# Optimization experiments

Hardware: AMD Instinct MI355X
Metric: run time of the kernel (lower is better)

## Reference

```python
import jax, jax.numpy as jnp
import numpy as np

B, S, D = 4, 2048, 1024          # batch, seq, hidden_units
E, K, I = 16, 2, 1024            # n_routed_experts, top_k, moe_inter_dim
SH = 2                            # n_shared_experts -> shared inter = SH*I
ROUTE_SCALE = 1.0


def setup_inputs() -> dict:
    key = jax.random.key(0)
    ks = jax.random.split(key, 12)
    std = 0.02
    return {
        "x": jax.random.normal(ks[0], (B, S, D), jnp.float32),
        "gate_w": jax.random.normal(ks[1], (E, D), jnp.float32) * std,
        # expert weights, torch Linear layout [out, in], stacked over experts
        "w1": jax.random.normal(ks[2], (E, I, D), jnp.float32) * std,
        "w2": jax.random.normal(ks[3], (E, D, I), jnp.float32) * std,
        "w3": jax.random.normal(ks[4], (E, I, D), jnp.float32) * std,
        # shared expert MLP (bias=True, nn.Linear default)
        "sw1": jax.random.normal(ks[5], (SH * I, D), jnp.float32) * std,
        "sb1": jnp.zeros((SH * I,), jnp.float32),
        "sw2": jax.random.normal(ks[6], (D, SH * I), jnp.float32) * std,
        "sb2": jnp.zeros((D,), jnp.float32),
        "sw3": jax.random.normal(ks[7], (SH * I, D), jnp.float32) * std,
        "sb3": jnp.zeros((SH * I,), jnp.float32),
    }


def reference(x, gate_w, w1, w2, w3, sw1, sb1, sw2, sb2, sw3, sb3):
    orig_shape = x.shape
    xt = x.reshape(-1, D)                       # [T, D]
    T = xt.shape[0]

    # ---- Gate: sigmoid scores, top-k, normalized weights ----
    scores = jax.nn.sigmoid(xt @ gate_w.T)      # [T, E]
    topk_vals, topk_idx = jax.lax.top_k(scores, K)
    weights = topk_vals / topk_vals.sum(-1, keepdims=True) * ROUTE_SCALE  # [T, K]

    # dense per-token-per-expert combine weight (zero for unselected experts)
    onehot = jax.nn.one_hot(topk_idx, E, dtype=xt.dtype)  # [T, K, E]
    w_full = jnp.einsum('tk,tke->te', weights, onehot)    # [T, E]

    # ---- Routed experts: SwiGLU per expert, weighted combine ----
    y = jnp.zeros_like(xt)
    for e in range(E):  # fixed small structural loop over experts
        h = jax.nn.silu(xt @ w1[e].T) * (xt @ w3[e].T)    # [T, I]
        y = y + w_full[:, e:e + 1] * (h @ w2[e].T)

    # ---- Load-balancing auxiliary loss ----
    counts = jax.lax.stop_gradient(onehot.sum((0, 1)))    # tokens per expert (non-diff, as in torch)
    expert_probs = w_full.sum(0)                          # sum of routing weights per expert
    f_i = E * counts / (K * T)
    P_i = expert_probs / T
    L_ExpBal = (f_i * P_i).sum()

    # ---- Shared expert (dense SwiGLU MLP with bias) ----
    z = (jax.nn.silu(xt @ sw1.T + sb1) * (xt @ sw3.T + sb3)) @ sw2.T + sb2

    return (y + z).reshape(orig_shape), L_ExpBal
```

## Files before the change

kernel.cpp:

```cpp
#include <hip/hip_runtime.h>
#include <cstdint>
#include <cstddef>

typedef unsigned short ushort_t;
typedef __attribute__((ext_vector_type(8))) short bf16x8;
typedef __attribute__((ext_vector_type(8))) unsigned short u16x8;
typedef __attribute__((ext_vector_type(4))) float f32x4;

#define T_TOKENS 8192
#define DIM      1024
#define NEXP     16

static __device__ __forceinline__ unsigned short f2bf(float f) {
  union { float f; unsigned u; } v; v.f = f;
  unsigned r = v.u + 0x7FFFu + ((v.u >> 16) & 1u);
  return (unsigned short)(r >> 16);
}

static __device__ __forceinline__ void gload16(const void* g, void* l) {
  __builtin_amdgcn_global_load_lds(
      (const __attribute__((address_space(1))) unsigned int*)g,
      (__attribute__((address_space(3))) unsigned int*)l, 16, 0, 0);
}

static __device__ __forceinline__ void xcd_map(int bx, int by, int gy,
                                               int& rb, int& cb) {
  int lin = bx + (by << 6);
  int xcd = lin & 7;
  int c = lin >> 3;
  int gyd = gy >> 3;
  cb = xcd * gyd + (c >> 6);
  rb = c & 63;
}

__global__ __launch_bounds__(256) void k_cvt8(const float* __restrict__ in,
                                              ushort_t* __restrict__ outp) {
  size_t i = ((size_t)blockIdx.x * 256 + threadIdx.x) * 8;
  float4 a = *(const float4*)(in + i);
  float4 b = *(const float4*)(in + i + 4);
  u16x8 o;
  o[0]=f2bf(a.x); o[1]=f2bf(a.y); o[2]=f2bf(a.z); o[3]=f2bf(a.w);
  o[4]=f2bf(b.x); o[5]=f2bf(b.y); o[6]=f2bf(b.z); o[7]=f2bf(b.w);
  *(u16x8*)(outp + i) = o;
}

__global__ __launch_bounds__(64) void k_score(const float* __restrict__ x,
                                              const float* __restrict__ gw,
                                              int* __restrict__ sel0,
                                              int* __restrict__ sel1,
                                              float* __restrict__ w0o,
                                              float* __restrict__ w1o) {
  int t = blockIdx.x;
  int lane = threadIdx.x;
  float xv[16];
  const float* xr = x + (size_t)t * DIM + lane * 16;
#pragma unroll
  for (int j = 0; j < 16; j += 4) {
    float4 v = *(const float4*)(xr + j);
    xv[j] = v.x; xv[j+1] = v.y; xv[j+2] = v.z; xv[j+3] = v.w;
  }
  float sc[NEXP];
#pragma unroll
  for (int e = 0; e < NEXP; e++) {
    const float* gr = gw + (size_t)e * DIM + lane * 16;
    float a = 0.f;
#pragma unroll
    for (int j = 0; j < 16; j += 4) {
      float4 g = *(const float4*)(gr + j);
      a += xv[j]*g.x + xv[j+1]*g.y + xv[j+2]*g.z + xv[j+3]*g.w;
    }
#pragma unroll
    for (int o = 32; o > 0; o >>= 1) a += __shfl_xor(a, o, 64);
    sc[e] = 1.f / (1.f + expf(-a));
  }
  if (lane == 0) {
    float best = -1e30f, sec = -1e30f;
    int bi = 0, si = 0;
#pragma unroll
    for (int e = 0; e < NEXP; e++) {
      float s = sc[e];
      if (s > best) { sec = best; si = bi; best = s; bi = e; }
      else if (s > sec) { sec = s; si = e; }
    }
    float inv = 1.f / (best + sec);
    sel0[t] = bi; sel1[t] = si;
    w0o[t] = best * inv; w1o[t] = sec * inv;
  }
}

__global__ __launch_bounds__(256) void k_compact(const int* __restrict__ sel0,
                                                 const int* __restrict__ sel1,
                                                 const float* __restrict__ w0v,
                                                 const float* __restrict__ w1v,
                                                 int* __restrict__ toklist,
                                                 float* __restrict__ wlist,
                                                 int* __restrict__ cnt,
                                                 float* __restrict__ probs) {
  const int e = blockIdx.x;
  const int tid = threadIdx.x;
  const int lane = tid & 63, wv = tid >> 6;
  __shared__ int wbase[4];
  __shared__ int woff[4];
  __shared__ int base;
  __shared__ float pacc[4];
  if (tid == 0) base = 0;
  float myprob = 0.f;
  int* tl = toklist + e * T_TOKENS;
  float* wl = wlist + e * T_TOKENS;
  __syncthreads();
  for (int t0 = 0; t0 < T_TOKENS; t0 += 256) {
    int t = t0 + tid;
    bool m0 = (sel0[t] == e), m1 = (sel1[t] == e);
    bool m = m0 || m1;
    float wgt = m0 ? w0v[t] : (m1 ? w1v[t] : 0.f);
    unsigned long long bal = __ballot(m);
    int prefix = __popcll(bal & ((1ull << lane) - 1ull));
    if (lane == 0) wbase[wv] = __popcll(bal);
    __syncthreads();
    if (tid == 0) {
      int a = base;
#pragma unroll
      for (int i = 0; i < 4; i++) { woff[i] = a; a += wbase[i]; }
      base = a;
    }
    __syncthreads();
    if (m) {
      int pos = woff[wv] + prefix;
      tl[pos] = t;
      wl[pos] = wgt;
    }
    myprob += wgt;
  }
#pragma unroll
  for (int o = 32; o > 0; o >>= 1) myprob += __shfl_xor(myprob, o, 64);
  if (lane == 0) pacc[wv] = myprob;
  __syncthreads();
  if (tid == 0) {
    cnt[e] = base;
    probs[e] = pacc[0] + pacc[1] + pacc[2] + pacc[3];
  }
}

__global__ void k_offsets(const int* __restrict__ cnt, const float* __restrict__ probs,
                          int* __restrict__ seg, float* __restrict__ loss_out) {
  if (threadIdx.x == 0 && blockIdx.x == 0) {
    int acc = 0;
    float L = 0.f;
    for (int e = 0; e < NEXP; e++) {
      seg[e] = acc; acc += cnt[e];
      float f = 16.f * (float)cnt[e] / (2.f * 8192.f);
      L += f * (probs[e] / 8192.f);
    }
    seg[NEXP] = acc;
    *loss_out = L;
  }
}

__global__ __launch_bounds__(256, 3) void k_gemm1(
    const ushort_t* __restrict__ X,
    const ushort_t* __restrict__ W1b, const ushort_t* __restrict__ W3b,
    const float* __restrict__ b1, const float* __restrict__ b3,
    ushort_t* __restrict__ P, int ldP,
    const int* __restrict__ toklist, const int* __restrict__ cnt,
    const int* __restrict__ seg) {
  __shared__ __align__(16) ushort_t As[2 * 4096];
  __shared__ __align__(16) ushort_t B1s[2 * 2048];
  __shared__ __align__(16) ushort_t B3s[2 * 2048];

  const int tid = threadIdx.x;
  const int lane = tid & 63, wave = tid >> 6;
  const int wm = wave >> 1, wn = wave & 1;
  int rb, cb;
  xcd_map(blockIdx.x, blockIdx.y, gridDim.y, rb, cb);
  const int e = blockIdx.z;

  int Ne, pbase;
  const int* tl = nullptr;
  const ushort_t* W1 = W1b;
  const ushort_t* W3 = W3b;
  if (cnt) {
    Ne = cnt[e];
    if (rb * 128 >= Ne) return;
    pbase = seg[e];
    tl = toklist + e * T_TOKENS;
    W1 += (size_t)e * 1024 * 1024;
    W3 += (size_t)e * 1024 * 1024;
  } else { Ne = T_TOKENS; pbase = 0; }

  const int c0 = wave * 2, c1 = c0 + 1;
  const int lrow = lane >> 2;
  const int lcol = (lane & 3) * 8;

  const int ar0 = rb * 128 + c0 * 16 + lrow;
  const int ar1 = rb * 128 + c1 * 16 + lrow;
  const int sr0 = tl ? tl[min(ar0, Ne - 1)] : ar0;
  const int sr1 = tl ? tl[min(ar1, Ne - 1)] : ar1;
  const ushort_t* apA0 = X + (size_t)sr0 * DIM + lcol;
  const ushort_t* apA1 = X + (size_t)sr1 * DIM + lcol;

  const int brw = cb * 64 + wave * 16 + lrow;
  const ushort_t* bp1 = W1 + (size_t)brw * DIM + lcol;
  const ushort_t* bp3 = W3 + (size_t)brw * DIM + lcol;

  const int o0 = c0 * 512, o1 = c1 * 512;
  const int ow = wave * 512;

  f32x4 acc1[4][2], acc3[4][2];
#pragma unroll
  for (int m = 0; m < 4; m++)
#pragma unroll
    for (int n = 0; n < 2; n++) {
      acc1[m][n] = (f32x4){0.f, 0.f, 0.f, 0.f};
      acc3[m][n] = (f32x4){0.f, 0.f, 0.f, 0.f};
    }

  const int koff = (lane >> 4) * 8;

#define STAGE1(AB, BB, K0) { \
    gload16(apA0 + (K0), As  + (AB) + o0); \
    gload16(apA1 + (K0), As  + (AB) + o1); \
    gload16(bp1  + (K0), B1s + (BB) + ow); \
    gload16(bp3  + (K0), B3s + (BB) + ow); }

#define PHASE1(AC, BC, T, STG) { \
    if (STG) STAGE1(4096 - (AC), 2048 - (BC), ((T) + 1) * 32); \
    bf16x8 af[4], b1f[2], b3f[2]; \
    _Pragma("unroll") \
    for (int m = 0; m < 4; m++) { \
      int row = wm * 64 + m * 16 + (lane & 15); \
      af[m] = *(const bf16x8*)(As + (AC) + row * 32 + koff); } \
    _Pragma("unroll") \
    for (int n = 0; n < 2; n++) { \
      int rw = wn * 32 + n * 16 + (lane & 15); \
      b1f[n] = *(const bf16x8*)(B1s + (BC) + rw * 32 + koff); \
      b3f[n] = *(const bf16x8*)(B3s + (BC) + rw * 32 + koff); } \
    _Pragma("unroll") \
    for (int m = 0; m < 4; m++) \
      _Pragma("unroll") \
      for (int n = 0; n < 2; n++) { \
        acc1[m][n] = __builtin_amdgcn_mfma_f32_16x16x32_bf16(af[m], b1f[n], acc1[m][n], 0, 0, 0); \
        acc3[m][n] = __builtin_amdgcn_mfma_f32_16x16x32_bf16(af[m], b3f[n], acc3[m][n], 0, 0, 0); } \
    __syncthreads(); }

  STAGE1(0, 0, 0);
  __syncthreads();
  for (int kk = 0; kk < 30; kk += 2) {
    PHASE1(0, 0, kk, 1);
    PHASE1(4096, 2048, kk + 1, 1);
  }
  PHASE1(0, 0, 30, 1);
  PHASE1(4096, 2048, 31, 0);
#undef PHASE1
#undef STAGE1

#pragma unroll
  for (int n = 0; n < 2; n++) {
    int col = cb * 64 + wn * 32 + n * 16 + (lane & 15);
    float bb1 = b1 ? b1[col] : 0.f;
    float bb3 = b3 ? b3[col] : 0.f;
#pragma unroll
    for (int m = 0; m < 4; m++) {
#pragma unroll
      for (int r = 0; r < 4; r++) {
        int row = rb * 128 + wm * 64 + m * 16 + (lane >> 4) * 4 + r;
        if (row < Ne) {
          float h1 = acc1[m][n][r] + bb1;
          float h3 = acc3[m][n][r] + bb3;
          float pv = (h1 / (1.f + expf(-h1))) * h3;
          P[(size_t)(pbase + row) * ldP + col] = f2bf(pv);
        }
      }
    }
  }
}

__global__ __launch_bounds__(256, 3) void k_gemm2(
    const ushort_t* __restrict__ Pbuf, const ushort_t* __restrict__ W2b,
    const float* __restrict__ b2,
    float* __restrict__ outp,
    const int* __restrict__ toklist, const float* __restrict__ wlist,
    const int* __restrict__ cnt, const int* __restrict__ seg, int Kd) {
  __shared__ __align__(16) ushort_t As[2 * 4096];
  __shared__ __align__(16) ushort_t Bs[2 * 4096];

  const int tid = threadIdx.x;
  const int lane = tid & 63, wave = tid >> 6;
  const int wm = wave >> 1, wn = wave & 1;
  int rb, cb;
  xcd_map(blockIdx.x, blockIdx.y, gridDim.y, rb, cb);
  const int e = blockIdx.z;

  int Ne;
  const ushort_t* A;
  const ushort_t* W2 = W2b;
  const int* tl = nullptr; const float* wl = nullptr;
  if (cnt) {
    Ne = cnt[e];
    if (rb * 128 >= Ne) return;
    A = Pbuf + (size_t)seg[e] * Kd;
    W2 += (size_t)e * 1024 * Kd;
    tl = toklist + e * T_TOKENS;
    wl = wlist + e * T_TOKENS;
  } else { Ne = T_TOKENS; A = Pbuf; }

  const int c0 = wave * 2, c1 = c0 + 1;
  const int lrow = lane >> 2;
  const int lcol = (lane & 3) * 8;

  const int sr0 = min(rb * 128 + c0 * 16 + lrow, Ne - 1);
  const int sr1 = min(rb * 128 + c1 * 16 + lrow, Ne - 1);
  const ushort_t* apA0 = A + (size_t)sr0 * Kd + lcol;
  const ushort_t* apA1 = A + (size_t)sr1 * Kd + lcol;

  const int br0 = cb * 128 + c0 * 16 + lrow;
  const int br1 = cb * 128 + c1 * 16 + lrow;
  const ushort_t* bp0 = W2 + (size_t)br0 * Kd + lcol;
  const ushort_t* bp1 = W2 + (size_t)br1 * Kd + lcol;

  const int o0 = c0 * 512, o1 = c1 * 512;

  f32x4 acc[4][4];
#pragma unroll
  for (int m = 0; m < 4; m++)
#pragma unroll
    for (int n = 0; n < 4; n++) acc[m][n] = (f32x4){0.f, 0.f, 0.f, 0.f};

  const int koff = (lane >> 4) * 8;
  const int ksteps = Kd >> 5;

#define STAGE2(BUF, K0) { \
    gload16(apA0 + (K0), As + (BUF) + o0); \
    gload16(apA1 + (K0), As + (BUF) + o1); \
    gload16(bp0  + (K0), Bs + (BUF) + o0); \
    gload16(bp1  + (K0), Bs + (BUF) + o1); }

#define PHASE2(CUR, T, STG) { \
    if (STG) STAGE2(4096 - (CUR), ((T) + 1) * 32); \
    bf16x8 af[4], bf[4]; \
    _Pragma("unroll") \
    for (int m = 0; m < 4; m++) { \
      int row = wm * 64 + m * 16 + (lane & 15); \
      af[m] = *(const bf16x8*)(As + (CUR) + row * 32 + koff); } \
    _Pragma("unroll") \
    for (int n = 0; n < 4; n++) { \
      int rw = wn * 64 + n * 16 + (lane & 15); \
      bf[n] = *(const bf16x8*)(Bs + (CUR) + rw * 32 + koff); } \
    _Pragma("unroll") \
    for (int m = 0; m < 4; m++) \
      _Pragma("unroll") \
      for (int n = 0; n < 4; n++) \
        acc[m][n] = __builtin_amdgcn_mfma_f32_16x16x32_bf16(af[m], bf[n], acc[m][n], 0, 0, 0); \
    __syncthreads(); }

  STAGE2(0, 0);
  __syncthreads();
  for (int kk = 0; kk < ksteps - 2; kk += 2) {
    PHASE2(0, kk, 1);
    PHASE2(4096, kk + 1, 1);
  }
  PHASE2(0, ksteps - 2, 1);
  PHASE2(4096, ksteps - 1, 0);
#undef PHASE2
#undef STAGE2

#pragma unroll
  for (int n = 0; n < 4; n++) {
    int col = cb * 128 + wn * 64 + n * 16 + (lane & 15);
    float bias = b2 ? b2[col] : 0.f;
#pragma unroll
    for (int m = 0; m < 4; m++) {
#pragma unroll
      for (int r = 0; r < 4; r++) {
        int rl = rb * 128 + wm * 64 + m * 16 + (lane >> 4) * 4 + r;
        if (cnt) {
          if (rl < Ne) {
            int tok = tl[rl];
            float wgt = wl[rl];
            atomicAdd(outp + (size_t)tok * DIM + col, acc[m][n][r] * wgt);
          }
        } else {
          outp[(size_t)rl * DIM + col] = acc[m][n][r] + bias;
        }
      }
    }
  }
}

extern "C" void kernel_launch(void* const* d_in, const int* in_sizes, int n_in,
                              void* d_out, int out_size, void* d_ws, size_t ws_size,
                              hipStream_t stream) {
  const float* x   = (const float*)d_in[0];
  const float* gw  = (const float*)d_in[1];
  const float* w1  = (const float*)d_in[2];
  const float* w2  = (const float*)d_in[3];
  const float* w3  = (const float*)d_in[4];
  const float* sw1 = (const float*)d_in[5];
  const float* sb1 = (const float*)d_in[6];
  const float* sw2 = (const float*)d_in[7];
  const float* sb2 = (const float*)d_in[8];
  const float* sw3 = (const float*)d_in[9];
  const float* sb3 = (const float*)d_in[10];
  float* out  = (float*)d_out;
  float* loss = out + (size_t)T_TOKENS * DIM;

  const size_t NW = (size_t)NEXP * 1024 * 1024;
  const size_t NS = (size_t)2048 * 1024;

  char* w = (char*)d_ws;
  ushort_t* w1b  = (ushort_t*)w; w += NW * 2;
  ushort_t* w2b  = (ushort_t*)w; w += NW * 2;
  ushort_t* w3b  = (ushort_t*)w; w += NW * 2;
  ushort_t* sw1b = (ushort_t*)w; w += NS * 2;
  ushort_t* sw2b = (ushort_t*)w; w += NS * 2;
  ushort_t* sw3b = (ushort_t*)w; w += NS * 2;
  ushort_t* p_buf = (ushort_t*)w; w += (size_t)33554432 + 262144;
  ushort_t* x_bf  = (ushort_t*)w; w += (size_t)T_TOKENS * DIM * 2;
  int*   toklist  = (int*)w;      w += (size_t)NEXP * T_TOKENS * 4;
  float* wlist    = (float*)w;    w += (size_t)NEXP * T_TOKENS * 4;
  int*   sel0     = (int*)w;      w += (size_t)T_TOKENS * 4;
  int*   sel1     = (int*)w;      w += (size_t)T_TOKENS * 4;
  float* w0v      = (float*)w;    w += (size_t)T_TOKENS * 4;
  float* w1v      = (float*)w;    w += (size_t)T_TOKENS * 4;
  int*   cnt      = (int*)w;      w += 64;
  float* probs    = (float*)w;    w += 64;
  int*   seg      = (int*)w;      w += 128;

  k_cvt8<<<(T_TOKENS * DIM) / 2048, 256, 0, stream>>>(x, x_bf);
  k_cvt8<<<NW / 2048, 256, 0, stream>>>(w1, w1b);
  k_cvt8<<<NW / 2048, 256, 0, stream>>>(w2, w2b);
  k_cvt8<<<NW / 2048, 256, 0, stream>>>(w3, w3b);
  k_cvt8<<<NS / 2048, 256, 0, stream>>>(sw1, sw1b);
  k_cvt8<<<NS / 2048, 256, 0, stream>>>(sw2, sw2b);
  k_cvt8<<<NS / 2048, 256, 0, stream>>>(sw3, sw3b);

  k_score<<<T_TOKENS, 64, 0, stream>>>(x, gw, sel0, sel1, w0v, w1v);
  k_compact<<<NEXP, 256, 0, stream>>>(sel0, sel1, w0v, w1v,
                                      toklist, wlist, cnt, probs);
  k_offsets<<<1, 64, 0, stream>>>(cnt, probs, seg, loss);

  k_gemm1<<<dim3(64, 32, 1), 256, 0, stream>>>(x_bf, sw1b, sw3b, sb1, sb3,
                                               p_buf, 2048, nullptr, nullptr, nullptr);
  k_gemm2<<<dim3(64, 8, 1), 256, 0, stream>>>(p_buf, sw2b, sb2, out,
                                              nullptr, nullptr, nullptr, nullptr, 2048);

  k_gemm1<<<dim3(64, 16, NEXP), 256, 0, stream>>>(x_bf, w1b, w3b, nullptr, nullptr,
                                                  p_buf, 1024, toklist, cnt, seg);
  k_gemm2<<<dim3(64, 8, NEXP), 256, 0, stream>>>(p_buf, w2b, nullptr, out,
                                                 toklist, wlist, cnt, seg, 1024);
}
```

Baseline: 599.1 us.

## Double GEMM K-tile to 64 with XOR-swizzled LDS and batch score tokens per block

Both GEMM kernels now stage 64-wide K tiles instead of 32, so each tile is consumed in two MFMA half-steps per barrier. This halves the number of __syncthreads and pipeline iterations. The LDS layout gains an XOR swizzle on the 16-byte column chunk to avoid bank conflicts on the wider rows. LDS use doubles, so the occupancy hint drops from 3 to 2 blocks per CU. Separately, the scoring kernel packs four tokens (one per wave) into each 256-thread block, which cuts the launch block count.

```diff
diff --git a/kernel.cpp b/kernel.cpp
--- a/kernel.cpp
+++ b/kernel.cpp
@@ -44,14 +44,15 @@
   *(u16x8*)(outp + i) = o;
 }
 
-__global__ __launch_bounds__(64) void k_score(const float* __restrict__ x,
-                                              const float* __restrict__ gw,
-                                              int* __restrict__ sel0,
-                                              int* __restrict__ sel1,
-                                              float* __restrict__ w0o,
-                                              float* __restrict__ w1o) {
-  int t = blockIdx.x;
-  int lane = threadIdx.x;
+__global__ __launch_bounds__(256) void k_score(const float* __restrict__ x,
+                                               const float* __restrict__ gw,
+                                               int* __restrict__ sel0,
+                                               int* __restrict__ sel1,
+                                               float* __restrict__ w0o,
+                                               float* __restrict__ w1o) {
+  int lane = threadIdx.x & 63;
+  int wv = threadIdx.x >> 6;
+  int t = blockIdx.x * 4 + wv;
   float xv[16];
   const float* xr = x + (size_t)t * DIM + lane * 16;
 #pragma unroll
@@ -156,16 +157,17 @@
   }
 }
 
-__global__ __launch_bounds__(256, 3) void k_gemm1(
+
+__global__ __launch_bounds__(256, 2) void k_gemm1(
     const ushort_t* __restrict__ X,
     const ushort_t* __restrict__ W1b, const ushort_t* __restrict__ W3b,
     const float* __restrict__ b1, const float* __restrict__ b3,
     ushort_t* __restrict__ P, int ldP,
     const int* __restrict__ toklist, const int* __restrict__ cnt,
     const int* __restrict__ seg) {
-  __shared__ __align__(16) ushort_t As[2 * 4096];
-  __shared__ __align__(16) ushort_t B1s[2 * 2048];
-  __shared__ __align__(16) ushort_t B3s[2 * 2048];
+  __shared__ __align__(16) ushort_t As[2 * 8192];
+  __shared__ __align__(16) ushort_t B1s[2 * 4096];
+  __shared__ __align__(16) ushort_t B3s[2 * 4096];
 
   const int tid = threadIdx.x;
   const int lane = tid & 63, wave = tid >> 6;
@@ -187,23 +189,35 @@
     W3 += (size_t)e * 1024 * 1024;
   } else { Ne = T_TOKENS; pbase = 0; }
 
-  const int c0 = wave * 2, c1 = c0 + 1;
-  const int lrow = lane >> 2;
-  const int lcol = (lane & 3) * 8;
-
-  const int ar0 = rb * 128 + c0 * 16 + lrow;
-  const int ar1 = rb * 128 + c1 * 16 + lrow;
-  const int sr0 = tl ? tl[min(ar0, Ne - 1)] : ar0;
-  const int sr1 = tl ? tl[min(ar1, Ne - 1)] : ar1;
-  const ushort_t* apA0 = X + (size_t)sr0 * DIM + lcol;
-  const ushort_t* apA1 = X + (size_t)sr1 * DIM + lcol;
-
-  const int brw = cb * 64 + wave * 16 + lrow;
-  const ushort_t* bp1 = W1 + (size_t)brw * DIM + lcol;
-  const ushort_t* bp3 = W3 + (size_t)brw * DIM + lcol;
-
-  const int o0 = c0 * 512, o1 = c1 * 512;
-  const int ow = wave * 512;
+  const int lrow = lane >> 3;
+  const int scol = ((lane & 7) ^ lrow) * 8;
+
+  const int ca = wave * 4;
+  int ga0 = rb * 128 + (ca + 0) * 8 + lrow;
+  int ga1 = rb * 128 + (ca + 1) * 8 + lrow;
+  int ga2 = rb * 128 + (ca + 2) * 8 + lrow;
+  int ga3 = rb * 128 + (ca + 3) * 8 + lrow;
+  const int s0 = tl ? tl[min(ga0, Ne - 1)] : ga0;
+  const int s1 = tl ? tl[min(ga1, Ne - 1)] : ga1;
+  const int s2 = tl ? tl[min(ga2, Ne - 1)] : ga2;
+  const int s3 = tl ? tl[min(ga3, Ne - 1)] : ga3;
+  const ushort_t* apA0 = X + (size_t)s0 * DIM + scol;
+  const ushort_t* apA1 = X + (size_t)s1 * DIM + scol;
+  const ushort_t* apA2 = X + (size_t)s2 * DIM + scol;
+  const ushort_t* apA3 = X + (size_t)s3 * DIM + scol;
+  const int oa0 = (ca + 0) * 512, oa1 = (ca + 1) * 512;
+  const int oa2 = (ca + 2) * 512, oa3 = (ca + 3) * 512;
+
+  const int brw0 = cb * 64 + wave * 16 + lrow;
+  const int brw1 = brw0 + 8;
+  const ushort_t* bp10 = W1 + (size_t)brw0 * DIM + scol;
+  const ushort_t* bp11 = W1 + (size_t)brw1 * DIM + scol;
+  const ushort_t* bp30 = W3 + (size_t)brw0 * DIM + scol;
+  const ushort_t* bp31 = W3 + (size_t)brw1 * DIM + scol;
+  const int ob0 = (wave * 2) * 512, ob1 = (wave * 2 + 1) * 512;
+
+  const int ks0 = (((lane >> 4) + 0) ^ (lane & 7)) * 8;
+  const int ks1 = (((lane >> 4) + 4) ^ (lane & 7)) * 8;
 
   f32x4 acc1[4][2], acc3[4][2];
 #pragma unroll
@@ -214,43 +228,50 @@
       acc3[m][n] = (f32x4){0.f, 0.f, 0.f, 0.f};
     }
 
-  const int koff = (lane >> 4) * 8;
-
 #define STAGE1(AB, BB, K0) { \
-    gload16(apA0 + (K0), As  + (AB) + o0); \
-    gload16(apA1 + (K0), As  + (AB) + o1); \
-    gload16(bp1  + (K0), B1s + (BB) + ow); \
-    gload16(bp3  + (K0), B3s + (BB) + ow); }
-
-#define PHASE1(AC, BC, T, STG) { \
-    if (STG) STAGE1(4096 - (AC), 2048 - (BC), ((T) + 1) * 32); \
+    gload16(apA0 + (K0), As  + (AB) + oa0); \
+    gload16(apA1 + (K0), As  + (AB) + oa1); \
+    gload16(apA2 + (K0), As  + (AB) + oa2); \
+    gload16(apA3 + (K0), As  + (AB) + oa3); \
+    gload16(bp10 + (K0), B1s + (BB) + ob0); \
+    gload16(bp11 + (K0), B1s + (BB) + ob1); \
+    gload16(bp30 + (K0), B3s + (BB) + ob0); \
+    gload16(bp31 + (K0), B3s + (BB) + ob1); }
+
+#define HALF1(AC, BC, KS) { \
     bf16x8 af[4], b1f[2], b3f[2]; \
     _Pragma("unroll") \
     for (int m = 0; m < 4; m++) { \
       int row = wm * 64 + m * 16 + (lane & 15); \
-      af[m] = *(const bf16x8*)(As + (AC) + row * 32 + koff); } \
+      af[m] = *(const bf16x8*)(As + (AC) + row * 64 + (KS)); } \
     _Pragma("unroll") \
     for (int n = 0; n < 2; n++) { \
       int rw = wn * 32 + n * 16 + (lane & 15); \
-      b1f[n] = *(const bf16x8*)(B1s + (BC) + rw * 32 + koff); \
-      b3f[n] = *(const bf16x8*)(B3s + (BC) + rw * 32 + koff); } \
+      b1f[n] = *(const bf16x8*)(B1s + (BC) + rw * 64 + (KS)); \
+      b3f[n] = *(const bf16x8*)(B3s + (BC) + rw * 64 + (KS)); } \
     _Pragma("unroll") \
     for (int m = 0; m < 4; m++) \
       _Pragma("unroll") \
       for (int n = 0; n < 2; n++) { \
         acc1[m][n] = __builtin_amdgcn_mfma_f32_16x16x32_bf16(af[m], b1f[n], acc1[m][n], 0, 0, 0); \
-        acc3[m][n] = __builtin_amdgcn_mfma_f32_16x16x32_bf16(af[m], b3f[n], acc3[m][n], 0, 0, 0); } \
+        acc3[m][n] = __builtin_amdgcn_mfma_f32_16x16x32_bf16(af[m], b3f[n], acc3[m][n], 0, 0, 0); } }
+
+#define PHASE1(AC, BC, T, STG) { \
+    if (STG) STAGE1(8192 - (AC), 4096 - (BC), ((T) + 1) * 64); \
+    HALF1(AC, BC, ks0); \
+    HALF1(AC, BC, ks1); \
     __syncthreads(); }
 
   STAGE1(0, 0, 0);
   __syncthreads();
-  for (int kk = 0; kk < 30; kk += 2) {
+  for (int kk = 0; kk < 14; kk += 2) {
     PHASE1(0, 0, kk, 1);
-    PHASE1(4096, 2048, kk + 1, 1);
-  }
-  PHASE1(0, 0, 30, 1);
-  PHASE1(4096, 2048, 31, 0);
+    PHASE1(8192, 4096, kk + 1, 1);
+  }
+  PHASE1(0, 0, 14, 1);
+  PHASE1(8192, 4096, 15, 0);
 #undef PHASE1
+#undef HALF1
 #undef STAGE1
 
 #pragma unroll
@@ -274,14 +295,14 @@
   }
 }
 
-__global__ __launch_bounds__(256, 3) void k_gemm2(
+__global__ __launch_bounds__(256, 2) void k_gemm2(
     const ushort_t* __restrict__ Pbuf, const ushort_t* __restrict__ W2b,
     const float* __restrict__ b2,
     float* __restrict__ outp,
     const int* __restrict__ toklist, const float* __restrict__ wlist,
     const int* __restrict__ cnt, const int* __restrict__ seg, int Kd) {
-  __shared__ __align__(16) ushort_t As[2 * 4096];
-  __shared__ __align__(16) ushort_t Bs[2 * 4096];
+  __shared__ __align__(16) ushort_t As[2 * 8192];
+  __shared__ __align__(16) ushort_t Bs[2 * 8192];
 
   const int tid = threadIdx.x;
   const int lane = tid & 63, wave = tid >> 6;
@@ -303,21 +324,32 @@
     wl = wlist + e * T_TOKENS;
   } else { Ne = T_TOKENS; A = Pbuf; }
 
-  const int c0 = wave * 2, c1 = c0 + 1;
-  const int lrow = lane >> 2;
-  const int lcol = (lane & 3) * 8;
-
-  const int sr0 = min(rb * 128 + c0 * 16 + lrow, Ne - 1);
-  const int sr1 = min(rb * 128 + c1 * 16 + lrow, Ne - 1);
-  const ushort_t* apA0 = A + (size_t)sr0 * Kd + lcol;
-  const ushort_t* apA1 = A + (size_t)sr1 * Kd + lcol;
-
-  const int br0 = cb * 128 + c0 * 16 + lrow;
-  const int br1 = cb * 128 + c1 * 16 + lrow;
-  const ushort_t* bp0 = W2 + (size_t)br0 * Kd + lcol;
-  const ushort_t* bp1 = W2 + (size_t)br1 * Kd + lcol;
-
-  const int o0 = c0 * 512, o1 = c1 * 512;
+  const int lrow = lane >> 3;
+  const int scol = ((lane & 7) ^ lrow) * 8;
+
+  const int ca = wave * 4;
+  const int a0 = min(rb * 128 + (ca + 0) * 8 + lrow, Ne - 1);
+  const int a1 = min(rb * 128 + (ca + 1) * 8 + lrow, Ne - 1);
+  const int a2 = min(rb * 128 + (ca + 2) * 8 + lrow, Ne - 1);
+  const int a3 = min(rb * 128 + (ca + 3) * 8 + lrow, Ne - 1);
+  const ushort_t* apA0 = A + (size_t)a0 * Kd + scol;
+  const ushort_t* apA1 = A + (size_t)a1 * Kd + scol;
+  const ushort_t* apA2 = A + (size_t)a2 * Kd + scol;
+  const ushort_t* apA3 = A + (size_t)a3 * Kd + scol;
+  const int oa0 = (ca + 0) * 512, oa1 = (ca + 1) * 512;
+  const int oa2 = (ca + 2) * 512, oa3 = (ca + 3) * 512;
+
+  const int br0 = cb * 128 + (ca + 0) * 8 + lrow;
+  const int br1 = cb * 128 + (ca + 1) * 8 + lrow;
+  const int br2 = cb * 128 + (ca + 2) * 8 + lrow;
+  const int br3 = cb * 128 + (ca + 3) * 8 + lrow;
+  const ushort_t* bp0 = W2 + (size_t)br0 * Kd + scol;
+  const ushort_t* bp1 = W2 + (size_t)br1 * Kd + scol;
+  const ushort_t* bp2 = W2 + (size_t)br2 * Kd + scol;
+  const ushort_t* bp3 = W2 + (size_t)br3 * Kd + scol;
+
+  const int ks0 = (((lane >> 4) + 0) ^ (lane & 7)) * 8;
+  const int ks1 = (((lane >> 4) + 4) ^ (lane & 7)) * 8;
 
   f32x4 acc[4][4];
 #pragma unroll
@@ -325,42 +357,50 @@
 #pragma unroll
     for (int n = 0; n < 4; n++) acc[m][n] = (f32x4){0.f, 0.f, 0.f, 0.f};
 
-  const int koff = (lane >> 4) * 8;
-  const int ksteps = Kd >> 5;
+  const int ksteps = Kd >> 6;
 
 #define STAGE2(BUF, K0) { \
-    gload16(apA0 + (K0), As + (BUF) + o0); \
-    gload16(apA1 + (K0), As + (BUF) + o1); \
-    gload16(bp0  + (K0), Bs + (BUF) + o0); \
-    gload16(bp1  + (K0), Bs + (BUF) + o1); }
-
-#define PHASE2(CUR, T, STG) { \
-    if (STG) STAGE2(4096 - (CUR), ((T) + 1) * 32); \
+    gload16(apA0 + (K0), As + (BUF) + oa0); \
+    gload16(apA1 + (K0), As + (BUF) + oa1); \
+    gload16(apA2 + (K0), As + (BUF) + oa2); \
+    gload16(apA3 + (K0), As + (BUF) + oa3); \
+    gload16(bp0  + (K0), Bs + (BUF) + oa0); \
+    gload16(bp1  + (K0), Bs + (BUF) + oa1); \
+    gload16(bp2  + (K0), Bs + (BUF) + oa2); \
+    gload16(bp3  + (K0), Bs + (BUF) + oa3); }
+
+#define HALF2(CUR, KS) { \
     bf16x8 af[4], bf[4]; \
     _Pragma("unroll") \
     for (int m = 0; m < 4; m++) { \
       int row = wm * 64 + m * 16 + (lane & 15); \
-      af[m] = *(const bf16x8*)(As + (CUR) + row * 32 + koff); } \
+      af[m] = *(const bf16x8*)(As + (CUR) + row * 64 + (KS)); } \
     _Pragma("unroll") \
     for (int n = 0; n < 4; n++) { \
       int rw = wn * 64 + n * 16 + (lane & 15); \
-      bf[n] = *(const bf16x8*)(Bs + (CUR) + rw * 32 + koff); } \
+      bf[n] = *(const bf16x8*)(Bs + (CUR) + rw * 64 + (KS)); } \
     _Pragma("unroll") \
     for (int m = 0; m < 4; m++) \
       _Pragma("unroll") \
       for (int n = 0; n < 4; n++) \
-        acc[m][n] = __builtin_amdgcn_mfma_f32_16x16x32_bf16(af[m], bf[n], acc[m][n], 0, 0, 0); \
+        acc[m][n] = __builtin_amdgcn_mfma_f32_16x16x32_bf16(af[m], bf[n], acc[m][n], 0, 0, 0); }
+
+#define PHASE2(CUR, T, STG) { \
+    if (STG) STAGE2(8192 - (CUR), ((T) + 1) * 64); \
+    HALF2(CUR, ks0); \
+    HALF2(CUR, ks1); \
     __syncthreads(); }
 
   STAGE2(0, 0);
   __syncthreads();
   for (int kk = 0; kk < ksteps - 2; kk += 2) {
     PHASE2(0, kk, 1);
-    PHASE2(4096, kk + 1, 1);
+    PHASE2(8192, kk + 1, 1);
   }
   PHASE2(0, ksteps - 2, 1);
-  PHASE2(4096, ksteps - 1, 0);
+  PHASE2(8192, ksteps - 1, 0);
 #undef PHASE2
+#undef HALF2
 #undef STAGE2
 
 #pragma unroll
@@ -433,7 +473,7 @@
   k_cvt8<<<NS / 2048, 256, 0, stream>>>(sw2, sw2b);
   k_cvt8<<<NS / 2048, 256, 0, stream>>>(sw3, sw3b);
 
-  k_score<<<T_TOKENS, 64, 0, stream>>>(x, gw, sel0, sel1, w0v, w1v);
+  k_score<<<T_TOKENS / 4, 256, 0, stream>>>(x, gw, sel0, sel1, w0v, w1v);
   k_compact<<<NEXP, 256, 0, stream>>>(sel0, sel1, w0v, w1v,
                                       toklist, wlist, cnt, probs);
   k_offsets<<<1, 64, 0, stream>>>(cnt, probs, seg, loss);
```

Result: slower. 622.2 us (+3.9%).
